# Optimization experiments

Measured on AMD Instinct MI355X. Metric: run time of the kernel, lower is better.

Reference implementation:

```python
import jax, jax.numpy as jnp
import numpy as np

N, S, D, H = 2, 2048, 1024, 16
DH = D // H  # 64


def setup_inputs() -> dict:
    key = jax.random.key(0)
    ks = jax.random.split(key, 7)
    scale = 1.0 / np.sqrt(DH)  # ~nn.Linear default init range
    return {
        "sequences": jax.random.normal(ks[0], (N, S, D), dtype=jnp.float32),
        "Wq": jax.random.uniform(ks[1], (H, DH, DH), jnp.float32, -scale, scale),
        "bq": jax.random.uniform(ks[2], (H, DH), jnp.float32, -scale, scale),
        "Wk": jax.random.uniform(ks[3], (H, DH, DH), jnp.float32, -scale, scale),
        "bk": jax.random.uniform(ks[4], (H, DH), jnp.float32, -scale, scale),
        "Wv": jax.random.uniform(ks[5], (H, DH, DH), jnp.float32, -scale, scale),
        "bv": jax.random.uniform(ks[6], (H, DH), jnp.float32, -scale, scale),
    }


def reference(sequences, Wq, bq, Wk, bk, Wv, bv):
    n, s, d = sequences.shape
    x = sequences.reshape(n, s, H, DH)  # [N,S,H,Dh]
    # per-head Linear: y = x @ W^T + b, batched over heads
    q = jnp.einsum('nshd,hed->nshe', x, Wq) + bq  # [N,S,H,Dh]
    k = jnp.einsum('nshd,hed->nshe', x, Wk) + bk
    v = jnp.einsum('nshd,hed->nshe', x, Wv) + bv
    # attention: scores [N,H,S,S]
    scores = jnp.einsum('nqhd,nkhd->nhqk', q, k) / jnp.sqrt(jnp.float32(DH))
    w = jax.nn.softmax(scores, axis=-1)
    out = jnp.einsum('nhqk,nkhd->nqhd', w, v)  # [N,S,H,Dh]
    return out.reshape(n, s, d)
```

## Files before the change

### kernel.cpp

```cpp
#include <hip/hip_runtime.h>
#include <hip/hip_bf16.h>


#define NB 2
#define SS 2048
#define DM 1024
#define NH 16
#define DHd 64

typedef __attribute__((ext_vector_type(8))) short bf16x8;
typedef __attribute__((ext_vector_type(4))) float f32x4;

union U8 { bf16x8 v; unsigned short u[8]; };

__device__ __forceinline__ unsigned short f2b(float x) {
    __hip_bfloat16 h = __float2bfloat16(x);
    return *reinterpret_cast<unsigned short*>(&h);
}

__device__ __forceinline__ bf16x8 pack8(float4 a, float4 b) {
    U8 t;
    t.u[0] = f2b(a.x); t.u[1] = f2b(a.y); t.u[2] = f2b(a.z); t.u[3] = f2b(a.w);
    t.u[4] = f2b(b.x); t.u[5] = f2b(b.y); t.u[6] = f2b(b.z); t.u[7] = f2b(b.w);
    return t.v;
}

__device__ __forceinline__ int swz(int row, int ch) {
    return row * 64 + ((ch ^ (row & 7)) * 8);
}

__global__ __launch_bounds__(256) void qkv_proj(
    const float* __restrict__ seq,
    const float* __restrict__ Wq, const float* __restrict__ bq,
    const float* __restrict__ Wk, const float* __restrict__ bk,
    const float* __restrict__ Wv, const float* __restrict__ bv,
    unsigned short* __restrict__ Q, unsigned short* __restrict__ K,
    unsigned short* __restrict__ Vt)
{
    __shared__ unsigned short Xl[128 * 64];
    __shared__ unsigned short Wl[3 * 64 * 64];

    const int tid = threadIdx.x;
    const int wv = tid >> 6, L = tid & 63, lo = L & 15, qd = L >> 4;
    const int bi = blockIdx.x;
    const int nh = bi >> 4, sb = bi & 15;
    const int h = nh & (NH - 1), n = nh >> 4;
    const int s0 = sb * 128;

#pragma unroll
    for (int i = 0; i < 4; ++i) {
        int idx = tid + i * 256;
        int r = idx >> 3, ch = idx & 7;
        const float* src = seq + ((size_t)(n * SS + s0 + r)) * DM + h * DHd + ch * 8;
        float4 a = ((const float4*)src)[0];
        float4 b = ((const float4*)src)[1];
        *(bf16x8*)&Xl[swz(r, ch)] = pack8(a, b);
    }
#pragma unroll
    for (int i = 0; i < 6; ++i) {
        int idx = tid + i * 256;
        int mat = idx >> 9;
        int rem = idx & 511;
        int e = rem >> 3, ch = rem & 7;
        const float* Wm = (mat == 0) ? Wq : (mat == 1) ? Wk : Wv;
        const float* src = Wm + (size_t)(h * DHd + e) * DHd + ch * 8;
        float4 a = ((const float4*)src)[0];
        float4 b = ((const float4*)src)[1];
        *(bf16x8*)&Wl[mat * 4096 + swz(e, ch)] = pack8(a, b);
    }
    __syncthreads();

    bf16x8 xf[2][2];
#pragma unroll
    for (int st = 0; st < 2; ++st)
#pragma unroll
        for (int kt = 0; kt < 2; ++kt)
            xf[st][kt] = *(const bf16x8*)&Xl[swz(wv * 32 + st * 16 + lo, kt * 4 + qd)];

#pragma unroll
    for (int m2 = 0; m2 < 2; ++m2) {
        const unsigned short* Wb = &Wl[m2 * 4096];
        const float* bias = m2 ? bk : bq;
        unsigned short* O = m2 ? K : Q;
        const float sc = m2 ? 1.0f : 0.125f;

        f32x4 acc[4][2];
#pragma unroll
        for (int et = 0; et < 4; ++et) {
            float4 bb = *(const float4*)&bias[h * DHd + et * 16 + qd * 4];
#pragma unroll
            for (int st = 0; st < 2; ++st)
                acc[et][st] = (f32x4){bb.x, bb.y, bb.z, bb.w};
        }
#pragma unroll
        for (int et = 0; et < 4; ++et) {
            bf16x8 wf0 = *(const bf16x8*)&Wb[swz(et * 16 + lo, qd)];
            bf16x8 wf1 = *(const bf16x8*)&Wb[swz(et * 16 + lo, 4 + qd)];
#pragma unroll
            for (int st = 0; st < 2; ++st) {
                acc[et][st] = __builtin_amdgcn_mfma_f32_16x16x32_bf16(
                    wf0, xf[st][0], acc[et][st], 0, 0, 0);
                acc[et][st] = __builtin_amdgcn_mfma_f32_16x16x32_bf16(
                    wf1, xf[st][1], acc[et][st], 0, 0, 0);
            }
        }
#pragma unroll
        for (int et = 0; et < 4; ++et)
#pragma unroll
            for (int st = 0; st < 2; ++st) {
                int s = s0 + wv * 32 + st * 16 + lo;
                ushort4 w;
                w.x = f2b(acc[et][st][0] * sc); w.y = f2b(acc[et][st][1] * sc);
                w.z = f2b(acc[et][st][2] * sc); w.w = f2b(acc[et][st][3] * sc);
                *(ushort4*)&O[((size_t)nh * SS + s) * DHd + et * 16 + qd * 4] = w;
            }
    }

    {
        const unsigned short* Wb = &Wl[2 * 4096];
        float bvv[4];
#pragma unroll
        for (int et = 0; et < 4; ++et) bvv[et] = bv[h * DHd + et * 16 + lo];

        f32x4 acc[2][4];
#pragma unroll
        for (int st = 0; st < 2; ++st)
#pragma unroll
            for (int et = 0; et < 4; ++et)
                acc[st][et] = (f32x4){bvv[et], bvv[et], bvv[et], bvv[et]};
#pragma unroll
        for (int et = 0; et < 4; ++et) {
            bf16x8 wf0 = *(const bf16x8*)&Wb[swz(et * 16 + lo, qd)];
            bf16x8 wf1 = *(const bf16x8*)&Wb[swz(et * 16 + lo, 4 + qd)];
#pragma unroll
            for (int st = 0; st < 2; ++st) {
                acc[st][et] = __builtin_amdgcn_mfma_f32_16x16x32_bf16(
                    xf[st][0], wf0, acc[st][et], 0, 0, 0);
                acc[st][et] = __builtin_amdgcn_mfma_f32_16x16x32_bf16(
                    xf[st][1], wf1, acc[st][et], 0, 0, 0);
            }
        }
#pragma unroll
        for (int st = 0; st < 2; ++st)
#pragma unroll
            for (int et = 0; et < 4; ++et) {
                int e = et * 16 + lo;
                int s = s0 + wv * 32 + st * 16 + qd * 4;
                ushort4 w;
                w.x = f2b(acc[st][et][0]); w.y = f2b(acc[st][et][1]);
                w.z = f2b(acc[st][et][2]); w.w = f2b(acc[st][et][3]);
                *(ushort4*)&Vt[((size_t)nh * DHd + e) * SS + s] = w;
            }
    }
}

#define PSTR 72

__global__ __launch_bounds__(256) void attn(
    const unsigned short* __restrict__ Qg, const unsigned short* __restrict__ Kg,
    const unsigned short* __restrict__ Vg, float* __restrict__ out)
{
    __shared__ unsigned short Kl[64 * 64];
    __shared__ unsigned short Vl[64 * 64];
    __shared__ unsigned short Pl[4][32 * PSTR];

    const int tid = threadIdx.x;
    const int wv = tid >> 6, L = tid & 63, lo = L & 15, qd = L >> 4;
    const int bi = blockIdx.x;
    const int nh = bi >> 4, qblk = bi & 15;
    const int h = nh & (NH - 1), n = nh >> 4;
    const int q0 = qblk * 128 + wv * 32;

    const unsigned short* Qnh = Qg + (size_t)nh * SS * DHd;
    const unsigned short* Knh = Kg + (size_t)nh * SS * DHd;
    const unsigned short* Vnh = Vg + (size_t)nh * DHd * SS;

    bf16x8 qf[2][2];
#pragma unroll
    for (int ct = 0; ct < 2; ++ct)
#pragma unroll
        for (int kt = 0; kt < 2; ++kt)
            qf[ct][kt] = *(const bf16x8*)(Qnh + (size_t)(q0 + ct * 16 + lo) * DHd
                                          + kt * 32 + qd * 8);

    f32x4 oacc[4][2];
#pragma unroll
    for (int rt = 0; rt < 4; ++rt)
#pragma unroll
        for (int ct = 0; ct < 2; ++ct)
            oacc[rt][ct] = (f32x4){0.f, 0.f, 0.f, 0.f};

    float m[2] = {-1e30f, -1e30f}, l[2] = {0.f, 0.f};

    for (int kv0 = 0; kv0 < SS; kv0 += 64) {
        __syncthreads();
#pragma unroll
        for (int i = 0; i < 2; ++i) {
            int idx = tid + i * 256;
            int r = idx >> 3, ch = idx & 7;
            *(uint4*)&Kl[swz(r, ch)] =
                *(const uint4*)(Knh + (size_t)(kv0 + r) * DHd + ch * 8);
            *(uint4*)&Vl[swz(r, ch)] =
                *(const uint4*)(Vnh + (size_t)r * SS + kv0 + ch * 8);
        }
        __syncthreads();

        f32x4 sacc[4][2];
#pragma unroll
        for (int rt = 0; rt < 4; ++rt)
#pragma unroll
            for (int ct = 0; ct < 2; ++ct)
                sacc[rt][ct] = (f32x4){0.f, 0.f, 0.f, 0.f};
#pragma unroll
        for (int rt = 0; rt < 4; ++rt)
#pragma unroll
            for (int kt = 0; kt < 2; ++kt) {
                bf16x8 kf = *(const bf16x8*)&Kl[swz(rt * 16 + lo, kt * 4 + qd)];
#pragma unroll
                for (int ct = 0; ct < 2; ++ct)
                    sacc[rt][ct] = __builtin_amdgcn_mfma_f32_16x16x32_bf16(
                        kf, qf[ct][kt], sacc[rt][ct], 0, 0, 0);
            }

#pragma unroll
        for (int ct = 0; ct < 2; ++ct) {
            float mx = sacc[0][ct][0];
#pragma unroll
            for (int rt = 0; rt < 4; ++rt)
#pragma unroll
                for (int r = 0; r < 4; ++r)
                    mx = fmaxf(mx, sacc[rt][ct][r]);
            mx = fmaxf(mx, __shfl_xor(mx, 16, 64));
            mx = fmaxf(mx, __shfl_xor(mx, 32, 64));
            const float mo = m[ct];
            const float mn = fmaxf(mo, mx);
            const float corr = __expf(mo - mn);
            float rs = 0.f;
#pragma unroll
            for (int rt = 0; rt < 4; ++rt) {
                float p0 = __expf(sacc[rt][ct][0] - mn);
                float p1 = __expf(sacc[rt][ct][1] - mn);
                float p2 = __expf(sacc[rt][ct][2] - mn);
                float p3 = __expf(sacc[rt][ct][3] - mn);
                rs += (p0 + p1) + (p2 + p3);
                ushort4 w;
                w.x = f2b(p0); w.y = f2b(p1); w.z = f2b(p2); w.w = f2b(p3);
                *(ushort4*)&Pl[wv][(ct * 16 + lo) * PSTR + rt * 16 + qd * 4] = w;
            }
            rs += __shfl_xor(rs, 16, 64);
            rs += __shfl_xor(rs, 32, 64);
            l[ct] = l[ct] * corr + rs;
            m[ct] = mn;
#pragma unroll
            for (int rt = 0; rt < 4; ++rt)
#pragma unroll
                for (int r = 0; r < 4; ++r)
                    oacc[rt][ct][r] *= corr;
        }

#pragma unroll
        for (int kt = 0; kt < 2; ++kt) {
            bf16x8 pf[2];
#pragma unroll
            for (int ct = 0; ct < 2; ++ct)
                pf[ct] = *(const bf16x8*)&Pl[wv][(ct * 16 + lo) * PSTR
                                                 + kt * 32 + qd * 8];
#pragma unroll
            for (int rt = 0; rt < 4; ++rt) {
                bf16x8 vf = *(const bf16x8*)&Vl[swz(rt * 16 + lo, kt * 4 + qd)];
#pragma unroll
                for (int ct = 0; ct < 2; ++ct)
                    oacc[rt][ct] = __builtin_amdgcn_mfma_f32_16x16x32_bf16(
                        vf, pf[ct], oacc[rt][ct], 0, 0, 0);
            }
        }
    }

#pragma unroll
    for (int ct = 0; ct < 2; ++ct) {
        const float inv = 1.0f / l[ct];
        const int s = q0 + ct * 16 + lo;
#pragma unroll
        for (int rt = 0; rt < 4; ++rt) {
            float4 o;
            o.x = oacc[rt][ct][0] * inv; o.y = oacc[rt][ct][1] * inv;
            o.z = oacc[rt][ct][2] * inv; o.w = oacc[rt][ct][3] * inv;
            *(float4*)&out[((size_t)n * SS + s) * DM + h * DHd
                           + rt * 16 + qd * 4] = o;
        }
    }
}

extern "C" void kernel_launch(void* const* d_in, const int* in_sizes, int n_in,
                              void* d_out, int out_size, void* d_ws, size_t ws_size,
                              hipStream_t stream) {
    const float* seq = (const float*)d_in[0];
    const float* Wq  = (const float*)d_in[1];
    const float* bq  = (const float*)d_in[2];
    const float* Wk  = (const float*)d_in[3];
    const float* bk  = (const float*)d_in[4];
    const float* Wv  = (const float*)d_in[5];
    const float* bv  = (const float*)d_in[6];
    float* out = (float*)d_out;

    const size_t per = (size_t)NB * NH * SS * DHd;
    unsigned short* Q  = (unsigned short*)d_ws;
    unsigned short* K  = Q + per;
    unsigned short* Vt = K + per;

    qkv_proj<<<512, 256, 0, stream>>>(seq, Wq, bq, Wk, bk, Wv, bv, Q, K, Vt);
    attn<<<512, 256, 0, stream>>>(Q, K, Vt, out);
}
```

Baseline: 157.2 us.

## Split QKV projection per matrix, halve attention tile, use exp2 with lazy rescale

The QKV projection now launches one block per (matrix, head, seq-block), which triples the grid and cuts shared memory, at the cost of loading the X tile three times. The attention kernel handles 16 query rows per wave instead of 32, so the grid doubles to 1024 blocks. Each block still streams the full K/V, so global K/V traffic doubles while register use falls. Softmax folds log2(e) into the Q scale and uses exp2f. The output rescale is skipped when no row max changed, and the P buffer uses a swizzled layout instead of padding.

```diff
diff --git a/kernel.cpp b/kernel.cpp
--- a/kernel.cpp
+++ b/kernel.cpp
@@ -11,15 +11,18 @@
 typedef __attribute__((ext_vector_type(8))) short bf16x8;
 typedef __attribute__((ext_vector_type(4))) float f32x4;
 
-union U8 { bf16x8 v; unsigned short u[8]; };
-
 __device__ __forceinline__ unsigned short f2b(float x) {
     __hip_bfloat16 h = __float2bfloat16(x);
     return *reinterpret_cast<unsigned short*>(&h);
 }
 
+__device__ __forceinline__ ushort4 pack4f(float a, float b, float c, float d) {
+    ushort4 r; r.x = f2b(a); r.y = f2b(b); r.z = f2b(c); r.w = f2b(d);
+    return r;
+}
+
 __device__ __forceinline__ bf16x8 pack8(float4 a, float4 b) {
-    U8 t;
+    union { bf16x8 v; unsigned short u[8]; } t;
     t.u[0] = f2b(a.x); t.u[1] = f2b(a.y); t.u[2] = f2b(a.z); t.u[3] = f2b(a.w);
     t.u[4] = f2b(b.x); t.u[5] = f2b(b.y); t.u[6] = f2b(b.z); t.u[7] = f2b(b.w);
     return t.v;
@@ -28,6 +31,8 @@
 __device__ __forceinline__ int swz(int row, int ch) {
     return row * 64 + ((ch ^ (row & 7)) * 8);
 }
+
+#define QSCALE 0.18033688011112042f
 
 __global__ __launch_bounds__(256) void qkv_proj(
     const float* __restrict__ seq,
@@ -38,14 +43,18 @@
     unsigned short* __restrict__ Vt)
 {
     __shared__ unsigned short Xl[128 * 64];
-    __shared__ unsigned short Wl[3 * 64 * 64];
+    __shared__ unsigned short Wl[64 * 64];
 
     const int tid = threadIdx.x;
     const int wv = tid >> 6, L = tid & 63, lo = L & 15, qd = L >> 4;
-    const int bi = blockIdx.x;
-    const int nh = bi >> 4, sb = bi & 15;
+    const int mat = blockIdx.x >> 9;
+    const int rem = blockIdx.x & 511;
+    const int nh = rem >> 4, sb = rem & 15;
     const int h = nh & (NH - 1), n = nh >> 4;
     const int s0 = sb * 128;
+
+    const float* Wm = (mat == 0) ? Wq : (mat == 1) ? Wk : Wv;
+    const float* bm = (mat == 0) ? bq : (mat == 1) ? bk : bv;
 
 #pragma unroll
     for (int i = 0; i < 4; ++i) {
@@ -57,16 +66,13 @@
         *(bf16x8*)&Xl[swz(r, ch)] = pack8(a, b);
     }
 #pragma unroll
-    for (int i = 0; i < 6; ++i) {
+    for (int i = 0; i < 2; ++i) {
         int idx = tid + i * 256;
-        int mat = idx >> 9;
-        int rem = idx & 511;
-        int e = rem >> 3, ch = rem & 7;
-        const float* Wm = (mat == 0) ? Wq : (mat == 1) ? Wk : Wv;
+        int e = idx >> 3, ch = idx & 7;
         const float* src = Wm + (size_t)(h * DHd + e) * DHd + ch * 8;
         float4 a = ((const float4*)src)[0];
         float4 b = ((const float4*)src)[1];
-        *(bf16x8*)&Wl[mat * 4096 + swz(e, ch)] = pack8(a, b);
+        *(bf16x8*)&Wl[swz(e, ch)] = pack8(a, b);
     }
     __syncthreads();
 
@@ -77,25 +83,22 @@
         for (int kt = 0; kt < 2; ++kt)
             xf[st][kt] = *(const bf16x8*)&Xl[swz(wv * 32 + st * 16 + lo, kt * 4 + qd)];
 
-#pragma unroll
-    for (int m2 = 0; m2 < 2; ++m2) {
-        const unsigned short* Wb = &Wl[m2 * 4096];
-        const float* bias = m2 ? bk : bq;
-        unsigned short* O = m2 ? K : Q;
-        const float sc = m2 ? 1.0f : 0.125f;
+    if (mat < 2) {
+        unsigned short* O = mat ? K : Q;
+        const float sc = mat ? 1.0f : QSCALE;
 
         f32x4 acc[4][2];
 #pragma unroll
         for (int et = 0; et < 4; ++et) {
-            float4 bb = *(const float4*)&bias[h * DHd + et * 16 + qd * 4];
+            float4 bb = *(const float4*)&bm[h * DHd + et * 16 + qd * 4];
 #pragma unroll
             for (int st = 0; st < 2; ++st)
                 acc[et][st] = (f32x4){bb.x, bb.y, bb.z, bb.w};
         }
 #pragma unroll
         for (int et = 0; et < 4; ++et) {
-            bf16x8 wf0 = *(const bf16x8*)&Wb[swz(et * 16 + lo, qd)];
-            bf16x8 wf1 = *(const bf16x8*)&Wb[swz(et * 16 + lo, 4 + qd)];
+            bf16x8 wf0 = *(const bf16x8*)&Wl[swz(et * 16 + lo, qd)];
+            bf16x8 wf1 = *(const bf16x8*)&Wl[swz(et * 16 + lo, 4 + qd)];
 #pragma unroll
             for (int st = 0; st < 2; ++st) {
                 acc[et][st] = __builtin_amdgcn_mfma_f32_16x16x32_bf16(
@@ -109,18 +112,14 @@
 #pragma unroll
             for (int st = 0; st < 2; ++st) {
                 int s = s0 + wv * 32 + st * 16 + lo;
-                ushort4 w;
-                w.x = f2b(acc[et][st][0] * sc); w.y = f2b(acc[et][st][1] * sc);
-                w.z = f2b(acc[et][st][2] * sc); w.w = f2b(acc[et][st][3] * sc);
+                ushort4 w = pack4f(acc[et][st][0] * sc, acc[et][st][1] * sc,
+                                   acc[et][st][2] * sc, acc[et][st][3] * sc);
                 *(ushort4*)&O[((size_t)nh * SS + s) * DHd + et * 16 + qd * 4] = w;
             }
-    }
-
-    {
-        const unsigned short* Wb = &Wl[2 * 4096];
+    } else {
         float bvv[4];
 #pragma unroll
-        for (int et = 0; et < 4; ++et) bvv[et] = bv[h * DHd + et * 16 + lo];
+        for (int et = 0; et < 4; ++et) bvv[et] = bm[h * DHd + et * 16 + lo];
 
         f32x4 acc[2][4];
 #pragma unroll
@@ -130,8 +129,8 @@
                 acc[st][et] = (f32x4){bvv[et], bvv[et], bvv[et], bvv[et]};
 #pragma unroll
         for (int et = 0; et < 4; ++et) {
-            bf16x8 wf0 = *(const bf16x8*)&Wb[swz(et * 16 + lo, qd)];
-            bf16x8 wf1 = *(const bf16x8*)&Wb[swz(et * 16 + lo, 4 + qd)];
+            bf16x8 wf0 = *(const bf16x8*)&Wl[swz(et * 16 + lo, qd)];
+            bf16x8 wf1 = *(const bf16x8*)&Wl[swz(et * 16 + lo, 4 + qd)];
 #pragma unroll
             for (int st = 0; st < 2; ++st) {
                 acc[st][et] = __builtin_amdgcn_mfma_f32_16x16x32_bf16(
@@ -146,15 +145,12 @@
             for (int et = 0; et < 4; ++et) {
                 int e = et * 16 + lo;
                 int s = s0 + wv * 32 + st * 16 + qd * 4;
-                ushort4 w;
-                w.x = f2b(acc[st][et][0]); w.y = f2b(acc[st][et][1]);
-                w.z = f2b(acc[st][et][2]); w.w = f2b(acc[st][et][3]);
+                ushort4 w = pack4f(acc[st][et][0], acc[st][et][1],
+                                   acc[st][et][2], acc[st][et][3]);
                 *(ushort4*)&Vt[((size_t)nh * DHd + e) * SS + s] = w;
             }
     }
 }
-
-#define PSTR 72
 
 __global__ __launch_bounds__(256) void attn(
     const unsigned short* __restrict__ Qg, const unsigned short* __restrict__ Kg,
@@ -162,35 +158,29 @@
 {
     __shared__ unsigned short Kl[64 * 64];
     __shared__ unsigned short Vl[64 * 64];
-    __shared__ unsigned short Pl[4][32 * PSTR];
+    __shared__ unsigned short Pl[4][16 * 64];
 
     const int tid = threadIdx.x;
     const int wv = tid >> 6, L = tid & 63, lo = L & 15, qd = L >> 4;
     const int bi = blockIdx.x;
-    const int nh = bi >> 4, qblk = bi & 15;
+    const int nh = bi >> 5, qblk = bi & 31;
     const int h = nh & (NH - 1), n = nh >> 4;
-    const int q0 = qblk * 128 + wv * 32;
+    const int q0 = qblk * 64 + wv * 16;
 
     const unsigned short* Qnh = Qg + (size_t)nh * SS * DHd;
     const unsigned short* Knh = Kg + (size_t)nh * SS * DHd;
     const unsigned short* Vnh = Vg + (size_t)nh * DHd * SS;
 
-    bf16x8 qf[2][2];
-#pragma unroll
-    for (int ct = 0; ct < 2; ++ct)
-#pragma unroll
-        for (int kt = 0; kt < 2; ++kt)
-            qf[ct][kt] = *(const bf16x8*)(Qnh + (size_t)(q0 + ct * 16 + lo) * DHd
-                                          + kt * 32 + qd * 8);
-
-    f32x4 oacc[4][2];
-#pragma unroll
-    for (int rt = 0; rt < 4; ++rt)
-#pragma unroll
-        for (int ct = 0; ct < 2; ++ct)
-            oacc[rt][ct] = (f32x4){0.f, 0.f, 0.f, 0.f};
-
-    float m[2] = {-1e30f, -1e30f}, l[2] = {0.f, 0.f};
+    bf16x8 qf[2];
+#pragma unroll
+    for (int kt = 0; kt < 2; ++kt)
+        qf[kt] = *(const bf16x8*)(Qnh + (size_t)(q0 + lo) * DHd + kt * 32 + qd * 8);
+
+    f32x4 oacc[4];
+#pragma unroll
+    for (int rt = 0; rt < 4; ++rt) oacc[rt] = (f32x4){0.f, 0.f, 0.f, 0.f};
+
+    float m = -1e30f, l = 0.f;
 
     for (int kv0 = 0; kv0 < SS; kv0 += 64) {
         __syncthreads();
@@ -205,89 +195,73 @@
         }
         __syncthreads();
 
-        f32x4 sacc[4][2];
-#pragma unroll
-        for (int rt = 0; rt < 4; ++rt)
-#pragma unroll
-            for (int ct = 0; ct < 2; ++ct)
-                sacc[rt][ct] = (f32x4){0.f, 0.f, 0.f, 0.f};
+        f32x4 sacc[4];
+#pragma unroll
+        for (int rt = 0; rt < 4; ++rt) sacc[rt] = (f32x4){0.f, 0.f, 0.f, 0.f};
 #pragma unroll
         for (int rt = 0; rt < 4; ++rt)
 #pragma unroll
             for (int kt = 0; kt < 2; ++kt) {
                 bf16x8 kf = *(const bf16x8*)&Kl[swz(rt * 16 + lo, kt * 4 + qd)];
-#pragma unroll
-                for (int ct = 0; ct < 2; ++ct)
-                    sacc[rt][ct] = __builtin_amdgcn_mfma_f32_16x16x32_bf16(
-                        kf, qf[ct][kt], sacc[rt][ct], 0, 0, 0);
-            }
-
-#pragma unroll
-        for (int ct = 0; ct < 2; ++ct) {
-            float mx = sacc[0][ct][0];
+                sacc[rt] = __builtin_amdgcn_mfma_f32_16x16x32_bf16(
+                    kf, qf[kt], sacc[rt], 0, 0, 0);
+            }
+
+        float mx = sacc[0][0];
+#pragma unroll
+        for (int rt = 0; rt < 4; ++rt)
+#pragma unroll
+            for (int r = 0; r < 4; ++r) mx = fmaxf(mx, sacc[rt][r]);
+        mx = fmaxf(mx, __shfl_xor(mx, 16, 64));
+        mx = fmaxf(mx, __shfl_xor(mx, 32, 64));
+        const float mn = fmaxf(m, mx);
+        const bool up = __any(mn > m);
+
+        float rs = 0.f;
+#pragma unroll
+        for (int rt = 0; rt < 4; ++rt) {
+            float p0 = exp2f(sacc[rt][0] - mn);
+            float p1 = exp2f(sacc[rt][1] - mn);
+            float p2 = exp2f(sacc[rt][2] - mn);
+            float p3 = exp2f(sacc[rt][3] - mn);
+            rs += (p0 + p1) + (p2 + p3);
+            *(ushort4*)&Pl[wv][swz(lo, 2 * rt + (qd >> 1)) + (qd & 1) * 4] =
+                pack4f(p0, p1, p2, p3);
+        }
+        rs += __shfl_xor(rs, 16, 64);
+        rs += __shfl_xor(rs, 32, 64);
+
+        if (up) {
+            const float corr = exp2f(m - mn);
+            l *= corr;
 #pragma unroll
             for (int rt = 0; rt < 4; ++rt)
 #pragma unroll
-                for (int r = 0; r < 4; ++r)
-                    mx = fmaxf(mx, sacc[rt][ct][r]);
-            mx = fmaxf(mx, __shfl_xor(mx, 16, 64));
-            mx = fmaxf(mx, __shfl_xor(mx, 32, 64));
-            const float mo = m[ct];
-            const float mn = fmaxf(mo, mx);
-            const float corr = __expf(mo - mn);
-            float rs = 0.f;
-#pragma unroll
-            for (int rt = 0; rt < 4; ++rt) {
-                float p0 = __expf(sacc[rt][ct][0] - mn);
-                float p1 = __expf(sacc[rt][ct][1] - mn);
-                float p2 = __expf(sacc[rt][ct][2] - mn);
-                float p3 = __expf(sacc[rt][ct][3] - mn);
-                rs += (p0 + p1) + (p2 + p3);
-                ushort4 w;
-                w.x = f2b(p0); w.y = f2b(p1); w.z = f2b(p2); w.w = f2b(p3);
-                *(ushort4*)&Pl[wv][(ct * 16 + lo) * PSTR + rt * 16 + qd * 4] = w;
-            }
-            rs += __shfl_xor(rs, 16, 64);
-            rs += __shfl_xor(rs, 32, 64);
-            l[ct] = l[ct] * corr + rs;
-            m[ct] = mn;
-#pragma unroll
-            for (int rt = 0; rt < 4; ++rt)
-#pragma unroll
-                for (int r = 0; r < 4; ++r)
-                    oacc[rt][ct][r] *= corr;
-        }
+                for (int r = 0; r < 4; ++r) oacc[rt][r] *= corr;
+            m = mn;
+        }
+        l += rs;
 
 #pragma unroll
         for (int kt = 0; kt < 2; ++kt) {
-            bf16x8 pf[2];
-#pragma unroll
-            for (int ct = 0; ct < 2; ++ct)
-                pf[ct] = *(const bf16x8*)&Pl[wv][(ct * 16 + lo) * PSTR
-                                                 + kt * 32 + qd * 8];
+            bf16x8 pf = *(const bf16x8*)&Pl[wv][swz(lo, kt * 4 + qd)];
 #pragma unroll
             for (int rt = 0; rt < 4; ++rt) {
                 bf16x8 vf = *(const bf16x8*)&Vl[swz(rt * 16 + lo, kt * 4 + qd)];
-#pragma unroll
-                for (int ct = 0; ct < 2; ++ct)
-                    oacc[rt][ct] = __builtin_amdgcn_mfma_f32_16x16x32_bf16(
-                        vf, pf[ct], oacc[rt][ct], 0, 0, 0);
-            }
-        }
-    }
-
-#pragma unroll
-    for (int ct = 0; ct < 2; ++ct) {
-        const float inv = 1.0f / l[ct];
-        const int s = q0 + ct * 16 + lo;
-#pragma unroll
-        for (int rt = 0; rt < 4; ++rt) {
-            float4 o;
-            o.x = oacc[rt][ct][0] * inv; o.y = oacc[rt][ct][1] * inv;
-            o.z = oacc[rt][ct][2] * inv; o.w = oacc[rt][ct][3] * inv;
-            *(float4*)&out[((size_t)n * SS + s) * DM + h * DHd
-                           + rt * 16 + qd * 4] = o;
-        }
+                oacc[rt] = __builtin_amdgcn_mfma_f32_16x16x32_bf16(
+                    vf, pf, oacc[rt], 0, 0, 0);
+            }
+        }
+    }
+
+    const float inv = 1.0f / l;
+    const int s = q0 + lo;
+#pragma unroll
+    for (int rt = 0; rt < 4; ++rt) {
+        float4 o;
+        o.x = oacc[rt][0] * inv; o.y = oacc[rt][1] * inv;
+        o.z = oacc[rt][2] * inv; o.w = oacc[rt][3] * inv;
+        *(float4*)&out[((size_t)n * SS + s) * DM + h * DHd + rt * 16 + qd * 4] = o;
     }
 }
 
@@ -308,6 +282,6 @@
     unsigned short* K  = Q + per;
     unsigned short* Vt = K + per;
 
-    qkv_proj<<<512, 256, 0, stream>>>(seq, Wq, bq, Wk, bk, Wv, bv, Q, K, Vt);
-    attn<<<512, 256, 0, stream>>>(Q, K, Vt, out);
-}
+    qkv_proj<<<1536, 256, 0, stream>>>(seq, Wq, bq, Wk, bk, Wv, bv, Q, K, Vt);
+    attn<<<1024, 256, 0, stream>>>(Q, K, Vt, out);
+}
```

After: 176.4 us. 12.2% more time.

## Fuse QKV projection into attention kernel, recomputing K/V per tile

Applied to the files above, without the earlier changes.

Merges the projection and attention kernels into one. Each block computes its own Q tile and recomputes the K and V projections for every KV tile straight from the fp32 input, holding Wk and Wv fragments in registers, so the Q/K/Vt workspace round-trip and the second launch are removed. The change also folds log2(e) into the Q scale so exp2 can be used, skips the output rescale when no lane's row max increases, and swizzles the P buffer instead of padding it. In exchange, the K/V projection is redundantly recomputed by all 16 query blocks per head, fp32 input is re-read many times, and register pressure rises.

```diff
diff --git a/kernel.cpp b/kernel.cpp
--- a/kernel.cpp
+++ b/kernel.cpp
@@ -11,15 +11,20 @@
 typedef __attribute__((ext_vector_type(8))) short bf16x8;
 typedef __attribute__((ext_vector_type(4))) float f32x4;
 
-union U8 { bf16x8 v; unsigned short u[8]; };
-
 __device__ __forceinline__ unsigned short f2b(float x) {
     __hip_bfloat16 h = __float2bfloat16(x);
     return *reinterpret_cast<unsigned short*>(&h);
 }
 
-__device__ __forceinline__ bf16x8 pack8(float4 a, float4 b) {
-    U8 t;
+__device__ __forceinline__ ushort4 pack4f(float a, float b, float c, float d) {
+    ushort4 r; r.x = f2b(a); r.y = f2b(b); r.z = f2b(c); r.w = f2b(d);
+    return r;
+}
+
+__device__ __forceinline__ bf16x8 ld8(const float* p) {
+    float4 a = ((const float4*)p)[0];
+    float4 b = ((const float4*)p)[1];
+    union { bf16x8 v; unsigned short u[8]; } t;
     t.u[0] = f2b(a.x); t.u[1] = f2b(a.y); t.u[2] = f2b(a.z); t.u[3] = f2b(a.w);
     t.u[4] = f2b(b.x); t.u[5] = f2b(b.y); t.u[6] = f2b(b.z); t.u[7] = f2b(b.w);
     return t.v;
@@ -29,140 +34,18 @@
     return row * 64 + ((ch ^ (row & 7)) * 8);
 }
 
-__global__ __launch_bounds__(256) void qkv_proj(
+#define QSCALE 0.18033688011112042f
+
+__global__ __launch_bounds__(256) void mhsa(
     const float* __restrict__ seq,
     const float* __restrict__ Wq, const float* __restrict__ bq,
     const float* __restrict__ Wk, const float* __restrict__ bk,
     const float* __restrict__ Wv, const float* __restrict__ bv,
-    unsigned short* __restrict__ Q, unsigned short* __restrict__ K,
-    unsigned short* __restrict__ Vt)
-{
-    __shared__ unsigned short Xl[128 * 64];
-    __shared__ unsigned short Wl[3 * 64 * 64];
-
-    const int tid = threadIdx.x;
-    const int wv = tid >> 6, L = tid & 63, lo = L & 15, qd = L >> 4;
-    const int bi = blockIdx.x;
-    const int nh = bi >> 4, sb = bi & 15;
-    const int h = nh & (NH - 1), n = nh >> 4;
-    const int s0 = sb * 128;
-
-#pragma unroll
-    for (int i = 0; i < 4; ++i) {
-        int idx = tid + i * 256;
-        int r = idx >> 3, ch = idx & 7;
-        const float* src = seq + ((size_t)(n * SS + s0 + r)) * DM + h * DHd + ch * 8;
-        float4 a = ((const float4*)src)[0];
-        float4 b = ((const float4*)src)[1];
-        *(bf16x8*)&Xl[swz(r, ch)] = pack8(a, b);
-    }
-#pragma unroll
-    for (int i = 0; i < 6; ++i) {
-        int idx = tid + i * 256;
-        int mat = idx >> 9;
-        int rem = idx & 511;
-        int e = rem >> 3, ch = rem & 7;
-        const float* Wm = (mat == 0) ? Wq : (mat == 1) ? Wk : Wv;
-        const float* src = Wm + (size_t)(h * DHd + e) * DHd + ch * 8;
-        float4 a = ((const float4*)src)[0];
-        float4 b = ((const float4*)src)[1];
-        *(bf16x8*)&Wl[mat * 4096 + swz(e, ch)] = pack8(a, b);
-    }
-    __syncthreads();
-
-    bf16x8 xf[2][2];
-#pragma unroll
-    for (int st = 0; st < 2; ++st)
-#pragma unroll
-        for (int kt = 0; kt < 2; ++kt)
-            xf[st][kt] = *(const bf16x8*)&Xl[swz(wv * 32 + st * 16 + lo, kt * 4 + qd)];
-
-#pragma unroll
-    for (int m2 = 0; m2 < 2; ++m2) {
-        const unsigned short* Wb = &Wl[m2 * 4096];
-        const float* bias = m2 ? bk : bq;
-        unsigned short* O = m2 ? K : Q;
-        const float sc = m2 ? 1.0f : 0.125f;
-
-        f32x4 acc[4][2];
-#pragma unroll
-        for (int et = 0; et < 4; ++et) {
-            float4 bb = *(const float4*)&bias[h * DHd + et * 16 + qd * 4];
-#pragma unroll
-            for (int st = 0; st < 2; ++st)
-                acc[et][st] = (f32x4){bb.x, bb.y, bb.z, bb.w};
-        }
-#pragma unroll
-        for (int et = 0; et < 4; ++et) {
-            bf16x8 wf0 = *(const bf16x8*)&Wb[swz(et * 16 + lo, qd)];
-            bf16x8 wf1 = *(const bf16x8*)&Wb[swz(et * 16 + lo, 4 + qd)];
-#pragma unroll
-            for (int st = 0; st < 2; ++st) {
-                acc[et][st] = __builtin_amdgcn_mfma_f32_16x16x32_bf16(
-                    wf0, xf[st][0], acc[et][st], 0, 0, 0);
-                acc[et][st] = __builtin_amdgcn_mfma_f32_16x16x32_bf16(
-                    wf1, xf[st][1], acc[et][st], 0, 0, 0);
-            }
-        }
-#pragma unroll
-        for (int et = 0; et < 4; ++et)
-#pragma unroll
-            for (int st = 0; st < 2; ++st) {
-                int s = s0 + wv * 32 + st * 16 + lo;
-                ushort4 w;
-                w.x = f2b(acc[et][st][0] * sc); w.y = f2b(acc[et][st][1] * sc);
-                w.z = f2b(acc[et][st][2] * sc); w.w = f2b(acc[et][st][3] * sc);
-                *(ushort4*)&O[((size_t)nh * SS + s) * DHd + et * 16 + qd * 4] = w;
-            }
-    }
-
-    {
-        const unsigned short* Wb = &Wl[2 * 4096];
-        float bvv[4];
-#pragma unroll
-        for (int et = 0; et < 4; ++et) bvv[et] = bv[h * DHd + et * 16 + lo];
-
-        f32x4 acc[2][4];
-#pragma unroll
-        for (int st = 0; st < 2; ++st)
-#pragma unroll
-            for (int et = 0; et < 4; ++et)
-                acc[st][et] = (f32x4){bvv[et], bvv[et], bvv[et], bvv[et]};
-#pragma unroll
-        for (int et = 0; et < 4; ++et) {
-            bf16x8 wf0 = *(const bf16x8*)&Wb[swz(et * 16 + lo, qd)];
-            bf16x8 wf1 = *(const bf16x8*)&Wb[swz(et * 16 + lo, 4 + qd)];
-#pragma unroll
-            for (int st = 0; st < 2; ++st) {
-                acc[st][et] = __builtin_amdgcn_mfma_f32_16x16x32_bf16(
-                    xf[st][0], wf0, acc[st][et], 0, 0, 0);
-                acc[st][et] = __builtin_amdgcn_mfma_f32_16x16x32_bf16(
-                    xf[st][1], wf1, acc[st][et], 0, 0, 0);
-            }
-        }
-#pragma unroll
-        for (int st = 0; st < 2; ++st)
-#pragma unroll
-            for (int et = 0; et < 4; ++et) {
-                int e = et * 16 + lo;
-                int s = s0 + wv * 32 + st * 16 + qd * 4;
-                ushort4 w;
-                w.x = f2b(acc[st][et][0]); w.y = f2b(acc[st][et][1]);
-                w.z = f2b(acc[st][et][2]); w.w = f2b(acc[st][et][3]);
-                *(ushort4*)&Vt[((size_t)nh * DHd + e) * SS + s] = w;
-            }
-    }
-}
-
-#define PSTR 72
-
-__global__ __launch_bounds__(256) void attn(
-    const unsigned short* __restrict__ Qg, const unsigned short* __restrict__ Kg,
-    const unsigned short* __restrict__ Vg, float* __restrict__ out)
+    float* __restrict__ out)
 {
     __shared__ unsigned short Kl[64 * 64];
     __shared__ unsigned short Vl[64 * 64];
-    __shared__ unsigned short Pl[4][32 * PSTR];
+    __shared__ unsigned short Pl[4][32 * 64];
 
     const int tid = threadIdx.x;
     const int wv = tid >> 6, L = tid & 63, lo = L & 15, qd = L >> 4;
@@ -171,17 +54,68 @@
     const int h = nh & (NH - 1), n = nh >> 4;
     const int q0 = qblk * 128 + wv * 32;
 
-    const unsigned short* Qnh = Qg + (size_t)nh * SS * DHd;
-    const unsigned short* Knh = Kg + (size_t)nh * SS * DHd;
-    const unsigned short* Vnh = Vg + (size_t)nh * DHd * SS;
-
+    const float* Wqh = Wq + h * DHd * DHd;
+    const float* Wkh = Wk + h * DHd * DHd;
+    const float* Wvh = Wv + h * DHd * DHd;
+    const float* Xn  = seq + (size_t)n * SS * DM + h * DHd;
+
+    bf16x8 awk[4][2], bwv[4][2];
+#pragma unroll
+    for (int t = 0; t < 4; ++t)
+#pragma unroll
+        for (int kt = 0; kt < 2; ++kt) {
+            awk[t][kt] = ld8(Wkh + (t * 16 + lo) * DHd + kt * 32 + qd * 8);
+            bwv[t][kt] = ld8(Wvh + (t * 16 + lo) * DHd + kt * 32 + qd * 8);
+        }
+    float4 bkf[4];
+    float  bvf[4];
+#pragma unroll
+    for (int t = 0; t < 4; ++t) {
+        bkf[t] = *(const float4*)&bk[h * DHd + t * 16 + qd * 4];
+        bvf[t] = bv[h * DHd + t * 16 + lo];
+    }
+
+    {
+        bf16x8 bxq[2][2];
+#pragma unroll
+        for (int ct = 0; ct < 2; ++ct)
+#pragma unroll
+            for (int kt = 0; kt < 2; ++kt)
+                bxq[ct][kt] = ld8(Xn + (size_t)(q0 + ct * 16 + lo) * DM
+                                  + kt * 32 + qd * 8);
+        f32x4 qacc[4][2];
+#pragma unroll
+        for (int et = 0; et < 4; ++et) {
+            float4 bb = *(const float4*)&bq[h * DHd + et * 16 + qd * 4];
+#pragma unroll
+            for (int ct = 0; ct < 2; ++ct)
+                qacc[et][ct] = (f32x4){bb.x, bb.y, bb.z, bb.w};
+        }
+#pragma unroll
+        for (int et = 0; et < 4; ++et)
+#pragma unroll
+            for (int kt = 0; kt < 2; ++kt) {
+                bf16x8 awq = ld8(Wqh + (et * 16 + lo) * DHd + kt * 32 + qd * 8);
+#pragma unroll
+                for (int ct = 0; ct < 2; ++ct)
+                    qacc[et][ct] = __builtin_amdgcn_mfma_f32_16x16x32_bf16(
+                        awq, bxq[ct][kt], qacc[et][ct], 0, 0, 0);
+            }
+#pragma unroll
+        for (int et = 0; et < 4; ++et)
+#pragma unroll
+            for (int ct = 0; ct < 2; ++ct)
+                *(ushort4*)&Pl[wv][swz(ct * 16 + lo, et * 2 + (qd >> 1))
+                                   + (qd & 1) * 4] =
+                    pack4f(qacc[et][ct][0] * QSCALE, qacc[et][ct][1] * QSCALE,
+                           qacc[et][ct][2] * QSCALE, qacc[et][ct][3] * QSCALE);
+    }
     bf16x8 qf[2][2];
 #pragma unroll
     for (int ct = 0; ct < 2; ++ct)
 #pragma unroll
         for (int kt = 0; kt < 2; ++kt)
-            qf[ct][kt] = *(const bf16x8*)(Qnh + (size_t)(q0 + ct * 16 + lo) * DHd
-                                          + kt * 32 + qd * 8);
+            qf[ct][kt] = *(const bf16x8*)&Pl[wv][swz(ct * 16 + lo, kt * 4 + qd)];
 
     f32x4 oacc[4][2];
 #pragma unroll
@@ -189,20 +123,47 @@
 #pragma unroll
         for (int ct = 0; ct < 2; ++ct)
             oacc[rt][ct] = (f32x4){0.f, 0.f, 0.f, 0.f};
-
     float m[2] = {-1e30f, -1e30f}, l[2] = {0.f, 0.f};
 
     for (int kv0 = 0; kv0 < SS; kv0 += 64) {
+        bf16x8 xv[2];
+        const float* xrow = Xn + (size_t)(kv0 + wv * 16 + lo) * DM;
+#pragma unroll
+        for (int kt = 0; kt < 2; ++kt)
+            xv[kt] = ld8(xrow + kt * 32 + qd * 8);
+
         __syncthreads();
-#pragma unroll
-        for (int i = 0; i < 2; ++i) {
-            int idx = tid + i * 256;
-            int r = idx >> 3, ch = idx & 7;
-            *(uint4*)&Kl[swz(r, ch)] =
-                *(const uint4*)(Knh + (size_t)(kv0 + r) * DHd + ch * 8);
-            *(uint4*)&Vl[swz(r, ch)] =
-                *(const uint4*)(Vnh + (size_t)r * SS + kv0 + ch * 8);
-        }
+
+        f32x4 kacc[4];
+#pragma unroll
+        for (int et = 0; et < 4; ++et)
+            kacc[et] = (f32x4){bkf[et].x, bkf[et].y, bkf[et].z, bkf[et].w};
+#pragma unroll
+        for (int et = 0; et < 4; ++et)
+#pragma unroll
+            for (int kt = 0; kt < 2; ++kt)
+                kacc[et] = __builtin_amdgcn_mfma_f32_16x16x32_bf16(
+                    awk[et][kt], xv[kt], kacc[et], 0, 0, 0);
+#pragma unroll
+        for (int et = 0; et < 4; ++et)
+            *(ushort4*)&Kl[swz(wv * 16 + lo, et * 2 + (qd >> 1)) + (qd & 1) * 4] =
+                pack4f(kacc[et][0], kacc[et][1], kacc[et][2], kacc[et][3]);
+
+        f32x4 vacc[4];
+#pragma unroll
+        for (int dt = 0; dt < 4; ++dt)
+            vacc[dt] = (f32x4){bvf[dt], bvf[dt], bvf[dt], bvf[dt]};
+#pragma unroll
+        for (int dt = 0; dt < 4; ++dt)
+#pragma unroll
+            for (int kt = 0; kt < 2; ++kt)
+                vacc[dt] = __builtin_amdgcn_mfma_f32_16x16x32_bf16(
+                    xv[kt], bwv[dt][kt], vacc[dt], 0, 0, 0);
+#pragma unroll
+        for (int dt = 0; dt < 4; ++dt)
+            *(ushort4*)&Vl[swz(dt * 16 + lo, wv * 2 + (qd >> 1)) + (qd & 1) * 4] =
+                pack4f(vacc[dt][0], vacc[dt][1], vacc[dt][2], vacc[dt][3]);
+
         __syncthreads();
 
         f32x4 sacc[4][2];
@@ -228,34 +189,34 @@
 #pragma unroll
             for (int rt = 0; rt < 4; ++rt)
 #pragma unroll
-                for (int r = 0; r < 4; ++r)
-                    mx = fmaxf(mx, sacc[rt][ct][r]);
+                for (int r = 0; r < 4; ++r) mx = fmaxf(mx, sacc[rt][ct][r]);
             mx = fmaxf(mx, __shfl_xor(mx, 16, 64));
             mx = fmaxf(mx, __shfl_xor(mx, 32, 64));
-            const float mo = m[ct];
-            const float mn = fmaxf(mo, mx);
-            const float corr = __expf(mo - mn);
+            const float mn = fmaxf(m[ct], mx);
+            const bool up = __any(mn > m[ct]);
             float rs = 0.f;
 #pragma unroll
             for (int rt = 0; rt < 4; ++rt) {
-                float p0 = __expf(sacc[rt][ct][0] - mn);
-                float p1 = __expf(sacc[rt][ct][1] - mn);
-                float p2 = __expf(sacc[rt][ct][2] - mn);
-                float p3 = __expf(sacc[rt][ct][3] - mn);
+                float p0 = exp2f(sacc[rt][ct][0] - mn);
+                float p1 = exp2f(sacc[rt][ct][1] - mn);
+                float p2 = exp2f(sacc[rt][ct][2] - mn);
+                float p3 = exp2f(sacc[rt][ct][3] - mn);
                 rs += (p0 + p1) + (p2 + p3);
-                ushort4 w;
-                w.x = f2b(p0); w.y = f2b(p1); w.z = f2b(p2); w.w = f2b(p3);
-                *(ushort4*)&Pl[wv][(ct * 16 + lo) * PSTR + rt * 16 + qd * 4] = w;
+                *(ushort4*)&Pl[wv][swz(ct * 16 + lo, rt * 2 + (qd >> 1))
+                                   + (qd & 1) * 4] = pack4f(p0, p1, p2, p3);
             }
             rs += __shfl_xor(rs, 16, 64);
             rs += __shfl_xor(rs, 32, 64);
-            l[ct] = l[ct] * corr + rs;
-            m[ct] = mn;
-#pragma unroll
-            for (int rt = 0; rt < 4; ++rt)
-#pragma unroll
-                for (int r = 0; r < 4; ++r)
-                    oacc[rt][ct][r] *= corr;
+            if (up) {
+                const float corr = exp2f(m[ct] - mn);
+                l[ct] *= corr;
+#pragma unroll
+                for (int rt = 0; rt < 4; ++rt)
+#pragma unroll
+                    for (int r = 0; r < 4; ++r) oacc[rt][ct][r] *= corr;
+                m[ct] = mn;
+            }
+            l[ct] += rs;
         }
 
 #pragma unroll
@@ -263,8 +224,7 @@
             bf16x8 pf[2];
 #pragma unroll
             for (int ct = 0; ct < 2; ++ct)
-                pf[ct] = *(const bf16x8*)&Pl[wv][(ct * 16 + lo) * PSTR
-                                                 + kt * 32 + qd * 8];
+                pf[ct] = *(const bf16x8*)&Pl[wv][swz(ct * 16 + lo, kt * 4 + qd)];
 #pragma unroll
             for (int rt = 0; rt < 4; ++rt) {
                 bf16x8 vf = *(const bf16x8*)&Vl[swz(rt * 16 + lo, kt * 4 + qd)];
@@ -303,11 +263,5 @@
     const float* bv  = (const float*)d_in[6];
     float* out = (float*)d_out;
 
-    const size_t per = (size_t)NB * NH * SS * DHd;
-    unsigned short* Q  = (unsigned short*)d_ws;
-    unsigned short* K  = Q + per;
-    unsigned short* Vt = K + per;
-
-    qkv_proj<<<512, 256, 0, stream>>>(seq, Wq, bq, Wk, bk, Wv, bv, Q, K, Vt);
-    attn<<<512, 256, 0, stream>>>(Q, K, Vt, out);
-}
+    mhsa<<<512, 256, 0, stream>>>(seq, Wq, bq, Wk, bk, Wv, bv, out);
+}
```

Result: slower. 269.0 us (+71.1%).

## Widen attention KV tile to 128, use exp2 softmax and conditional rescale

Applied to the files above, without the earlier changes.

Doubles the KV tile per iteration from 64 to 128 keys, with larger K/V/P shared buffers and a new 16-chunk swizzle for V, which halves the number of loop iterations and barriers. Q is prescaled by log2(e)/sqrt(d) so the softmax can use exp2f. The output and sum correction is skipped when no row maximum in the wave increases. Blocks are reordered so consecutive blocks cover different heads. The larger tile raises register and LDS use, which may lower occupancy.

```diff
diff --git a/kernel.cpp b/kernel.cpp
--- a/kernel.cpp
+++ b/kernel.cpp
@@ -11,15 +11,18 @@
 typedef __attribute__((ext_vector_type(8))) short bf16x8;
 typedef __attribute__((ext_vector_type(4))) float f32x4;
 
-union U8 { bf16x8 v; unsigned short u[8]; };
-
 __device__ __forceinline__ unsigned short f2b(float x) {
     __hip_bfloat16 h = __float2bfloat16(x);
     return *reinterpret_cast<unsigned short*>(&h);
 }
 
+__device__ __forceinline__ ushort4 pack4f(float a, float b, float c, float d) {
+    ushort4 r; r.x = f2b(a); r.y = f2b(b); r.z = f2b(c); r.w = f2b(d);
+    return r;
+}
+
 __device__ __forceinline__ bf16x8 pack8(float4 a, float4 b) {
-    U8 t;
+    union { bf16x8 v; unsigned short u[8]; } t;
     t.u[0] = f2b(a.x); t.u[1] = f2b(a.y); t.u[2] = f2b(a.z); t.u[3] = f2b(a.w);
     t.u[4] = f2b(b.x); t.u[5] = f2b(b.y); t.u[6] = f2b(b.z); t.u[7] = f2b(b.w);
     return t.v;
@@ -28,6 +31,11 @@
 __device__ __forceinline__ int swz(int row, int ch) {
     return row * 64 + ((ch ^ (row & 7)) * 8);
 }
+__device__ __forceinline__ int swzV(int row, int ch) {
+    return row * 128 + ((ch ^ (row & 15)) * 8);
+}
+
+#define QSCALE 0.18033688011112042f
 
 __global__ __launch_bounds__(256) void qkv_proj(
     const float* __restrict__ seq,
@@ -82,7 +90,7 @@
         const unsigned short* Wb = &Wl[m2 * 4096];
         const float* bias = m2 ? bk : bq;
         unsigned short* O = m2 ? K : Q;
-        const float sc = m2 ? 1.0f : 0.125f;
+        const float sc = m2 ? 1.0f : QSCALE;
 
         f32x4 acc[4][2];
 #pragma unroll
@@ -109,9 +117,8 @@
 #pragma unroll
             for (int st = 0; st < 2; ++st) {
                 int s = s0 + wv * 32 + st * 16 + lo;
-                ushort4 w;
-                w.x = f2b(acc[et][st][0] * sc); w.y = f2b(acc[et][st][1] * sc);
-                w.z = f2b(acc[et][st][2] * sc); w.w = f2b(acc[et][st][3] * sc);
+                ushort4 w = pack4f(acc[et][st][0] * sc, acc[et][st][1] * sc,
+                                   acc[et][st][2] * sc, acc[et][st][3] * sc);
                 *(ushort4*)&O[((size_t)nh * SS + s) * DHd + et * 16 + qd * 4] = w;
             }
     }
@@ -146,28 +153,27 @@
             for (int et = 0; et < 4; ++et) {
                 int e = et * 16 + lo;
                 int s = s0 + wv * 32 + st * 16 + qd * 4;
-                ushort4 w;
-                w.x = f2b(acc[st][et][0]); w.y = f2b(acc[st][et][1]);
-                w.z = f2b(acc[st][et][2]); w.w = f2b(acc[st][et][3]);
+                ushort4 w = pack4f(acc[st][et][0], acc[st][et][1],
+                                   acc[st][et][2], acc[st][et][3]);
                 *(ushort4*)&Vt[((size_t)nh * DHd + e) * SS + s] = w;
             }
     }
 }
 
-#define PSTR 72
+#define PSTR 136
 
 __global__ __launch_bounds__(256) void attn(
     const unsigned short* __restrict__ Qg, const unsigned short* __restrict__ Kg,
     const unsigned short* __restrict__ Vg, float* __restrict__ out)
 {
-    __shared__ unsigned short Kl[64 * 64];
-    __shared__ unsigned short Vl[64 * 64];
+    __shared__ unsigned short Kl[128 * 64];
+    __shared__ unsigned short Vl[64 * 128];
     __shared__ unsigned short Pl[4][32 * PSTR];
 
     const int tid = threadIdx.x;
     const int wv = tid >> 6, L = tid & 63, lo = L & 15, qd = L >> 4;
     const int bi = blockIdx.x;
-    const int nh = bi >> 4, qblk = bi & 15;
+    const int nh = bi & 31, qblk = bi >> 5;
     const int h = nh & (NH - 1), n = nh >> 4;
     const int q0 = qblk * 128 + wv * 32;
 
@@ -192,27 +198,28 @@
 
     float m[2] = {-1e30f, -1e30f}, l[2] = {0.f, 0.f};
 
-    for (int kv0 = 0; kv0 < SS; kv0 += 64) {
+    for (int kv0 = 0; kv0 < SS; kv0 += 128) {
         __syncthreads();
 #pragma unroll
-        for (int i = 0; i < 2; ++i) {
+        for (int i = 0; i < 4; ++i) {
             int idx = tid + i * 256;
-            int r = idx >> 3, ch = idx & 7;
-            *(uint4*)&Kl[swz(r, ch)] =
-                *(const uint4*)(Knh + (size_t)(kv0 + r) * DHd + ch * 8);
-            *(uint4*)&Vl[swz(r, ch)] =
-                *(const uint4*)(Vnh + (size_t)r * SS + kv0 + ch * 8);
+            int rk = idx >> 3, chk = idx & 7;
+            *(uint4*)&Kl[swz(rk, chk)] =
+                *(const uint4*)(Knh + (size_t)(kv0 + rk) * DHd + chk * 8);
+            int rv = idx >> 4, chv = idx & 15;
+            *(uint4*)&Vl[swzV(rv, chv)] =
+                *(const uint4*)(Vnh + (size_t)rv * SS + kv0 + chv * 8);
         }
         __syncthreads();
 
-        f32x4 sacc[4][2];
-#pragma unroll
-        for (int rt = 0; rt < 4; ++rt)
+        f32x4 sacc[8][2];
+#pragma unroll
+        for (int rt = 0; rt < 8; ++rt)
 #pragma unroll
             for (int ct = 0; ct < 2; ++ct)
                 sacc[rt][ct] = (f32x4){0.f, 0.f, 0.f, 0.f};
 #pragma unroll
-        for (int rt = 0; rt < 4; ++rt)
+        for (int rt = 0; rt < 8; ++rt)
 #pragma unroll
             for (int kt = 0; kt < 2; ++kt) {
                 bf16x8 kf = *(const bf16x8*)&Kl[swz(rt * 16 + lo, kt * 4 + qd)];
@@ -226,48 +233,49 @@
         for (int ct = 0; ct < 2; ++ct) {
             float mx = sacc[0][ct][0];
 #pragma unroll
-            for (int rt = 0; rt < 4; ++rt)
+            for (int rt = 0; rt < 8; ++rt)
 #pragma unroll
                 for (int r = 0; r < 4; ++r)
                     mx = fmaxf(mx, sacc[rt][ct][r]);
             mx = fmaxf(mx, __shfl_xor(mx, 16, 64));
             mx = fmaxf(mx, __shfl_xor(mx, 32, 64));
-            const float mo = m[ct];
-            const float mn = fmaxf(mo, mx);
-            const float corr = __expf(mo - mn);
+            const float mn = fmaxf(m[ct], mx);
+            const bool up = __any(mn > m[ct]);
             float rs = 0.f;
 #pragma unroll
-            for (int rt = 0; rt < 4; ++rt) {
-                float p0 = __expf(sacc[rt][ct][0] - mn);
-                float p1 = __expf(sacc[rt][ct][1] - mn);
-                float p2 = __expf(sacc[rt][ct][2] - mn);
-                float p3 = __expf(sacc[rt][ct][3] - mn);
+            for (int rt = 0; rt < 8; ++rt) {
+                float p0 = exp2f(sacc[rt][ct][0] - mn);
+                float p1 = exp2f(sacc[rt][ct][1] - mn);
+                float p2 = exp2f(sacc[rt][ct][2] - mn);
+                float p3 = exp2f(sacc[rt][ct][3] - mn);
                 rs += (p0 + p1) + (p2 + p3);
-                ushort4 w;
-                w.x = f2b(p0); w.y = f2b(p1); w.z = f2b(p2); w.w = f2b(p3);
-                *(ushort4*)&Pl[wv][(ct * 16 + lo) * PSTR + rt * 16 + qd * 4] = w;
+                *(ushort4*)&Pl[wv][(ct * 16 + lo) * PSTR + rt * 16 + qd * 4] =
+                    pack4f(p0, p1, p2, p3);
             }
             rs += __shfl_xor(rs, 16, 64);
             rs += __shfl_xor(rs, 32, 64);
-            l[ct] = l[ct] * corr + rs;
-            m[ct] = mn;
-#pragma unroll
-            for (int rt = 0; rt < 4; ++rt)
-#pragma unroll
-                for (int r = 0; r < 4; ++r)
-                    oacc[rt][ct][r] *= corr;
-        }
-
-#pragma unroll
-        for (int kt = 0; kt < 2; ++kt) {
+            if (up) {
+                const float corr = exp2f(m[ct] - mn);
+                l[ct] *= corr;
+#pragma unroll
+                for (int rt = 0; rt < 4; ++rt)
+#pragma unroll
+                    for (int r = 0; r < 4; ++r) oacc[rt][ct][r] *= corr;
+                m[ct] = mn;
+            }
+            l[ct] += rs;
+        }
+
+#pragma unroll
+        for (int kt2 = 0; kt2 < 4; ++kt2) {
             bf16x8 pf[2];
 #pragma unroll
             for (int ct = 0; ct < 2; ++ct)
                 pf[ct] = *(const bf16x8*)&Pl[wv][(ct * 16 + lo) * PSTR
-                                                 + kt * 32 + qd * 8];
+                                                 + kt2 * 32 + qd * 8];
 #pragma unroll
             for (int rt = 0; rt < 4; ++rt) {
-                bf16x8 vf = *(const bf16x8*)&Vl[swz(rt * 16 + lo, kt * 4 + qd)];
+                bf16x8 vf = *(const bf16x8*)&Vl[swzV(rt * 16 + lo, kt2 * 4 + qd)];
 #pragma unroll
                 for (int ct = 0; ct < 2; ++ct)
                     oacc[rt][ct] = __builtin_amdgcn_mfma_f32_16x16x32_bf16(
```

Result: slower. 161.8 us (+2.9%).
